# Kernel optimization log

Measured on AMD Instinct MI355X. Metric: run time of the kernel, lower is better.

Reference implementation:

```python
import jax, jax.numpy as jnp
import numpy as np

N_NODES = 100000
N_EDGES = 1600000
IN_DIM = 128
HID = 128
FC_DIM = 64
OUT_DIM = 1
NUM_LAYERS = 8
NUM_GRAPHS = 128
EPS = 1e-5


def _layernorm(x, gamma, beta):
    mu = jnp.mean(x, axis=-1, keepdims=True)
    var = jnp.mean(jnp.square(x - mu), axis=-1, keepdims=True)
    return (x - mu) * jax.lax.rsqrt(var + EPS) * gamma + beta


def _gcn_conv(x, row, col, W, b):
    # PyG GCNConv: h = X W; out[v] = sum_{(u,v)} norm(u,v) h[u] + b
    # self-loops already appended to row/col, norms precomputable per call
    n = x.shape[0]
    deg = jnp.zeros((n,), x.dtype).at[col].add(jnp.ones((row.shape[0],), x.dtype))
    dinv = jnp.where(deg > 0, jax.lax.rsqrt(deg), 0.0)
    norm = dinv[row] * dinv[col]                      # [E+N]
    h = x @ W                                         # [N, H]
    out = jnp.zeros((n, W.shape[1]), x.dtype).at[col].add(norm[:, None] * h[row])
    return out + b


def _block(x, row, col, W, b, g, be):
    return jax.nn.relu(_layernorm(_gcn_conv(x, row, col, W, b), g, be))


def setup_inputs() -> dict:
    key = jax.random.key(0)
    ks = jax.random.split(key, 16)
    x = jax.random.normal(ks[0], (N_NODES, IN_DIM), jnp.float32)
    edge_index = jax.random.randint(ks[1], (2, N_EDGES), 0, N_NODES, jnp.int32)
    batch = jnp.sort(jax.random.randint(ks[2], (N_NODES,), 0, NUM_GRAPHS, jnp.int32))

    def lin(k, fan_in, fan_out):
        s = 1.0 / np.sqrt(fan_in)
        return jax.random.uniform(k, (fan_in, fan_out), jnp.float32, -s, s)

    return {
        "x": x, "edge_index": edge_index, "batch": batch,
        "W_in": lin(ks[3], IN_DIM, HID), "b_in": jnp.zeros((HID,), jnp.float32),
        "g_in": jnp.ones((HID,), jnp.float32), "be_in": jnp.zeros((HID,), jnp.float32),
        "W_mid": lin(ks[4], HID, HID), "b_mid": jnp.zeros((HID,), jnp.float32),
        "g_mid": jnp.ones((HID,), jnp.float32), "be_mid": jnp.zeros((HID,), jnp.float32),
        "W_out": lin(ks[5], HID, HID), "b_out": jnp.zeros((HID,), jnp.float32),
        "g_out": jnp.ones((HID,), jnp.float32), "be_out": jnp.zeros((HID,), jnp.float32),
        "W1": lin(ks[6], HID, FC_DIM), "b1": jnp.zeros((FC_DIM,), jnp.float32),
        "W2": lin(ks[7], FC_DIM, OUT_DIM), "b2": jnp.zeros((OUT_DIM,), jnp.float32),
    }


def reference(x, edge_index, batch,
              W_in, b_in, g_in, be_in,
              W_mid, b_mid, g_mid, be_mid,
              W_out, b_out, g_out, be_out,
              W1, b1, W2, b2):
    n = x.shape[0]
    sl = jnp.arange(n, dtype=edge_index.dtype)
    row = jnp.concatenate([edge_index[0], sl])   # sources (+ self loops)
    col = jnp.concatenate([edge_index[1], sl])   # targets (+ self loops)

    # layer 0
    h = _block(x, row, col, W_in, b_in, g_in, be_in)
    # layers 1..num_layers-2 share middle_conv params; even idx adds residual
    for i in range(1, NUM_LAYERS - 1):
        if i % 2 == 0:
            h = _block(h, row, col, W_mid, b_mid, g_mid, be_mid) + h
        else:
            h = _block(h, row, col, W_mid, b_mid, g_mid, be_mid)
    # last layer
    h = _block(h, row, col, W_out, b_out, g_out, be_out)

    # global mean pool over batch ids
    ones = jnp.ones((n, 1), h.dtype)
    sums = jnp.zeros((NUM_GRAPHS, HID), h.dtype).at[batch].add(h)
    cnts = jnp.zeros((NUM_GRAPHS, 1), h.dtype).at[batch].add(ones)
    pooled = sums / jnp.maximum(cnts, 1.0)

    z = jax.nn.relu(pooled @ W1 + b1)            # dropout = identity (eval)
    return jax.nn.sigmoid(z @ W2 + b2)
```

## Files before the change

### kernel.cpp

```cpp
#include <hip/hip_runtime.h>
#include <hip/hip_fp16.h>

#define NN 100000
#define NE 1600000
#define DIM 128
#define NGRAPH 128
#define FCD 64

#define NBK 391
#define ECH 8192
#define NCH 196
#define ECAP 8192

typedef _Float16 half_t;
typedef _Float16 half2_t __attribute__((ext_vector_type(2)));
typedef _Float16 half4_t __attribute__((ext_vector_type(4)));
typedef _Float16 half8_t __attribute__((ext_vector_type(8)));
typedef float float4_t __attribute__((ext_vector_type(4)));

__device__ inline half2_t u2h(unsigned u) { union { unsigned u; half2_t h; } x; x.u = u; return x.h; }
__device__ inline unsigned h2u(half2_t h) { union { unsigned u; half2_t h; } x; x.h = h; return x.u; }
__device__ inline half8_t q2h8(uint4 q) { union { uint4 q; half8_t h; } x; x.q = q; return x.h; }

__global__ __launch_bounds__(256) void k_bucketA(const int* __restrict__ row,
                                                 const int* __restrict__ col,
                                                 int* __restrict__ staged,
                                                 int* __restrict__ offmat,
                                                 int* __restrict__ gtot) {
  __shared__ int hist[NBK];
  __shared__ int sc[512];
  __shared__ int off[NBK + 1];
  __shared__ int fill[NBK];
  int b = blockIdx.x, t = threadIdx.x;
  int e0 = b * ECH;
  int n = NE - e0; if (n > ECH) n = ECH;
  for (int j = t; j < NBK; j += 256) { hist[j] = 0; fill[j] = 0; }
  __syncthreads();
  for (int i = t; i < n; i += 256) atomicAdd(&hist[col[e0 + i] >> 8], 1);
  __syncthreads();
  sc[t] = (t < NBK) ? hist[t] : 0;
  sc[t + 256] = (t + 256 < NBK) ? hist[t + 256] : 0;
  __syncthreads();
  #pragma unroll
  for (int o = 1; o < 512; o <<= 1) {
    int a0 = (t >= o) ? sc[t - o] : 0;
    int a1 = (t + 256 >= o) ? sc[t + 256 - o] : 0;
    __syncthreads();
    sc[t] += a0; sc[t + 256] += a1;
    __syncthreads();
  }
  if (t == 0) off[0] = 0;
  for (int j = t; j < NBK; j += 256) off[j + 1] = sc[j];
  for (int j = t; j < NBK; j += 256) if (hist[j]) atomicAdd(&gtot[j], hist[j]);
  __syncthreads();
  for (int j = t; j < NBK + 1; j += 256) offmat[b * (NBK + 1) + j] = off[j];
  for (int i = t; i < n; i += 256) {
    int c = col[e0 + i], r = row[e0 + i];
    int bkt = c >> 8;
    int pos = off[bkt] + atomicAdd(&fill[bkt], 1);
    staged[e0 + pos] = (r << 8) | (c & 255);
  }
}

__global__ void k_bsum(const int* __restrict__ gtot, int* __restrict__ gbase,
                       int* __restrict__ rowptr) {
  __shared__ int sc[512];
  int t = threadIdx.x;
  sc[t] = (t < NBK) ? gtot[t] : 0;
  sc[t + 256] = (t + 256 < NBK) ? gtot[t + 256] : 0;
  __syncthreads();
  #pragma unroll
  for (int o = 1; o < 512; o <<= 1) {
    int a0 = (t >= o) ? sc[t - o] : 0;
    int a1 = (t + 256 >= o) ? sc[t + 256 - o] : 0;
    __syncthreads();
    sc[t] += a0; sc[t + 256] += a1;
    __syncthreads();
  }
  if (t == 0) { gbase[0] = 0; rowptr[NN] = NE; }
  for (int j = t; j < NBK; j += 256) gbase[j + 1] = sc[j];
}

__global__ __launch_bounds__(256) void k_csrB(const int* __restrict__ staged,
                                              const int* __restrict__ offmat,
                                              const int* __restrict__ gbase,
                                              int* __restrict__ rowptr,
                                              float* __restrict__ dinv,
                                              int* __restrict__ csrc) {
  __shared__ int pay[ECAP];
  __shared__ int csn[256];
  __shared__ int nhist[256];
  __shared__ int nscan[256];
  __shared__ int nb[256];
  __shared__ int nfill[256];
  int bkt = blockIdx.x, t = threadIdx.x;
  int gb = gbase[bkt];
  int off = 0, cnt = 0;
  if (t < NCH) {
    int base = t * (NBK + 1) + bkt;
    off = offmat[base];
    cnt = offmat[base + 1] - off;
  }
  csn[t] = cnt;
  __syncthreads();
  #pragma unroll
  for (int o = 1; o < 256; o <<= 1) {
    int a = (t >= o) ? csn[t - o] : 0;
    __syncthreads();
    csn[t] += a;
    __syncthreads();
  }
  int lb = csn[t] - cnt;
  int total = csn[255];
  if (t < NCH) {
    const int* src = staged + t * ECH + off;
    for (int i = 0; i < cnt; i++) pay[lb + i] = src[i];
  }
  nhist[t] = 0; nfill[t] = 0;
  __syncthreads();
  for (int i = t; i < total; i += 256) atomicAdd(&nhist[pay[i] & 255], 1);
  __syncthreads();
  nscan[t] = nhist[t];
  __syncthreads();
  #pragma unroll
  for (int o = 1; o < 256; o <<= 1) {
    int a = (t >= o) ? nscan[t - o] : 0;
    __syncthreads();
    nscan[t] += a;
    __syncthreads();
  }
  nb[t] = nscan[t] - nhist[t];
  int v = bkt * 256 + t;
  if (v < NN) {
    rowptr[v] = gb + nb[t];
    dinv[v] = rsqrtf((float)(nhist[t] + 1));
  }
  __syncthreads();
  for (int i = t; i < total; i += 256) {
    int p = pay[i];
    int cl = p & 255;
    int pos = nb[cl] + atomicAdd(&nfill[cl], 1);
    csrc[gb + pos] = p >> 8;
  }
}

__global__ void k_cvt(const float* __restrict__ x, half_t* __restrict__ Xh) {
  int i = blockIdx.x * 256 + threadIdx.x;
  if ((size_t)i * 4 < (size_t)NN * DIM) {
    float4 v = *(const float4*)&x[(size_t)i * 4];
    half4_t h; h[0] = (half_t)v.x; h[1] = (half_t)v.y; h[2] = (half_t)v.z; h[3] = (half_t)v.w;
    *(half4_t*)&Xh[(size_t)i * 4] = h;
  }
}

__global__ void k_wt(const float* __restrict__ W, half_t* __restrict__ Wt) {
  int e = blockIdx.x * 256 + threadIdx.x;
  if (e < DIM * DIM) {
    int j = e >> 7, k = e & 127;
    Wt[e] = (half_t)W[k * DIM + j];
  }
}

#define WT_DW 66
__global__ __launch_bounds__(256) void k_gemm(const half_t* __restrict__ X,
                                              const uint4* __restrict__ Wtg,
                                              const float* __restrict__ dinv,
                                              half_t* __restrict__ O) {
  __shared__ unsigned wt[DIM * WT_DW];
  __shared__ half_t outs[4][16 * 136];
  int t = threadIdx.x;
  int w = t >> 6, l = t & 63;
  #pragma unroll
  for (int i = 0; i < 8; i++) {
    int e = t + i * 256;
    int j = e >> 4, seg = e & 15;
    *(uint4*)&wt[j * WT_DW + seg * 4] = Wtg[e];
  }
  __syncthreads();
  int lr = l & 15, lk = l >> 4;
  #pragma unroll
  for (int t4 = 0; t4 < 2; t4++) {
    int n0w = blockIdx.x * 128 + w * 32 + t4 * 16;
    int nA = n0w + lr;
    uint4 a0 = make_uint4(0,0,0,0), a1 = a0, a2 = a0, a3 = a0;
    if (nA < NN) {
      const uint4* Xq = (const uint4*)&X[(size_t)nA * DIM];
      a0 = Xq[lk];  a1 = Xq[4 + lk];  a2 = Xq[8 + lk];  a3 = Xq[12 + lk];
    }
    float4_t acc[8] = {};
    #pragma unroll
    for (int jt = 0; jt < 8; jt++) {
      int bbase = (jt * 16 + lr) * WT_DW + lk * 4;
      uint4 b0 = *(const uint4*)&wt[bbase];
      uint4 b1 = *(const uint4*)&wt[bbase + 16];
      uint4 b2 = *(const uint4*)&wt[bbase + 32];
      uint4 b3 = *(const uint4*)&wt[bbase + 48];
      acc[jt] = __builtin_amdgcn_mfma_f32_16x16x32_f16(q2h8(a0), q2h8(b0), acc[jt], 0, 0, 0);
      acc[jt] = __builtin_amdgcn_mfma_f32_16x16x32_f16(q2h8(a1), q2h8(b1), acc[jt], 0, 0, 0);
      acc[jt] = __builtin_amdgcn_mfma_f32_16x16x32_f16(q2h8(a2), q2h8(b2), acc[jt], 0, 0, 0);
      acc[jt] = __builtin_amdgcn_mfma_f32_16x16x32_f16(q2h8(a3), q2h8(b3), acc[jt], 0, 0, 0);
    }
    float dv0 = dinv[min(n0w + lk * 4 + 0, NN - 1)];
    float dv1 = dinv[min(n0w + lk * 4 + 1, NN - 1)];
    float dv2 = dinv[min(n0w + lk * 4 + 2, NN - 1)];
    float dv3 = dinv[min(n0w + lk * 4 + 3, NN - 1)];
    #pragma unroll
    for (int jt = 0; jt < 8; jt++) {
      int cb = jt * 16 + lr;
      outs[w][(lk * 4 + 0) * 136 + cb] = (half_t)(acc[jt][0] * dv0);
      outs[w][(lk * 4 + 1) * 136 + cb] = (half_t)(acc[jt][1] * dv1);
      outs[w][(lk * 4 + 2) * 136 + cb] = (half_t)(acc[jt][2] * dv2);
      outs[w][(lk * 4 + 3) * 136 + cb] = (half_t)(acc[jt][3] * dv3);
    }
    #pragma unroll
    for (int q = 0; q < 4; q++) {
      int idx = l * 4 + q;
      int row = idx >> 4, seg = idx & 15;
      int n = n0w + row;
      if (n < NN) {
        uint4 o4 = *(const uint4*)&outs[w][row * 136 + seg * 8];
        *(uint4*)&O[(size_t)n * DIM + seg * 8] = o4;
      }
    }
  }
}

__global__ __launch_bounds__(256) void k_agg(const half2_t* __restrict__ Hh,
                      half2_t* __restrict__ Ah,
                      const int* __restrict__ rowptr, const int* __restrict__ csrc,
                      const float* __restrict__ dinv,
                      const float* __restrict__ bias, const float* __restrict__ gamma,
                      const float* __restrict__ beta, int res) {
  int tid = threadIdx.x;
  int lane = tid & 63;
  int v = blockIdx.x * 4 + (tid >> 6);
  int g = lane >> 4;
  int fl = lane & 15;
  int s0 = rowptr[v];
  int cnt = rowptr[v + 1] - s0;
  const uint4* Hq = (const uint4*)Hh;
  half2_t a0 = u2h(0u), a1 = u2h(0u), a2 = u2h(0u), a3 = u2h(0u);
  for (int i = g; i < cnt; i += 16) {
    int j1 = i + 4, j2 = i + 8, j3 = i + 12;
    int c1 = min(j1, cnt - 1);
    int c2 = min(j2, cnt - 1);
    int c3 = min(j3, cnt - 1);
    int e0 = csrc[s0 + i];
    int e1 = csrc[s0 + c1];
    int e2 = csrc[s0 + c2];
    int e3 = csrc[s0 + c3];
    uint4 q0 = Hq[(size_t)e0 * 16 + fl];
    uint4 q1 = Hq[(size_t)e1 * 16 + fl];
    uint4 q2 = Hq[(size_t)e2 * 16 + fl];
    uint4 q3 = Hq[(size_t)e3 * 16 + fl];
    a0 += u2h(q0.x); a1 += u2h(q0.y); a2 += u2h(q0.z); a3 += u2h(q0.w);
    if (j1 < cnt) { a0 += u2h(q1.x); a1 += u2h(q1.y); a2 += u2h(q1.z); a3 += u2h(q1.w); }
    if (j2 < cnt) { a0 += u2h(q2.x); a1 += u2h(q2.y); a2 += u2h(q2.z); a3 += u2h(q2.w); }
    if (j3 < cnt) { a0 += u2h(q3.x); a1 += u2h(q3.y); a2 += u2h(q3.z); a3 += u2h(q3.w); }
  }
  float f0 = (float)a0[0], f1 = (float)a0[1], f2 = (float)a1[0], f3 = (float)a1[1];
  float f4 = (float)a2[0], f5 = (float)a2[1], f6 = (float)a3[0], f7 = (float)a3[1];
  f0 += __shfl_xor(f0, 16); f0 += __shfl_xor(f0, 32);
  f1 += __shfl_xor(f1, 16); f1 += __shfl_xor(f1, 32);
  f2 += __shfl_xor(f2, 16); f2 += __shfl_xor(f2, 32);
  f3 += __shfl_xor(f3, 16); f3 += __shfl_xor(f3, 32);
  f4 += __shfl_xor(f4, 16); f4 += __shfl_xor(f4, 32);
  f5 += __shfl_xor(f5, 16); f5 += __shfl_xor(f5, 32);
  f6 += __shfl_xor(f6, 16); f6 += __shfl_xor(f6, 32);
  f7 += __shfl_xor(f7, 16); f7 += __shfl_xor(f7, 32);
  uint4 qs = Hq[(size_t)v * 16 + fl];
  half2_t s0h = u2h(qs.x), s1h = u2h(qs.y), s2h = u2h(qs.z), s3h = u2h(qs.w);
  f0 += (float)s0h[0]; f1 += (float)s0h[1]; f2 += (float)s1h[0]; f3 += (float)s1h[1];
  f4 += (float)s2h[0]; f5 += (float)s2h[1]; f6 += (float)s3h[0]; f7 += (float)s3h[1];
  float dv = dinv[v];
  float4 ba = *(const float4*)&bias[fl * 8];
  float4 bb = *(const float4*)&bias[fl * 8 + 4];
  f0 = f0 * dv + ba.x; f1 = f1 * dv + ba.y; f2 = f2 * dv + ba.z; f3 = f3 * dv + ba.w;
  f4 = f4 * dv + bb.x; f5 = f5 * dv + bb.y; f6 = f6 * dv + bb.z; f7 = f7 * dv + bb.w;
  float s  = ((f0 + f1) + (f2 + f3)) + ((f4 + f5) + (f6 + f7));
  float ss = ((f0 * f0 + f1 * f1) + (f2 * f2 + f3 * f3))
           + ((f4 * f4 + f5 * f5) + (f6 * f6 + f7 * f7));
  #pragma unroll
  for (int o = 1; o < 16; o <<= 1) { s += __shfl_xor(s, o); ss += __shfl_xor(ss, o); }
  float mu = s * (1.f / 128.f);
  float var = ss * (1.f / 128.f) - mu * mu;
  float rs = rsqrtf(var + 1e-5f);
  float pa = (g == 0) ? f0 : (g == 1) ? f2 : (g == 2) ? f4 : f6;
  float pb = (g == 0) ? f1 : (g == 1) ? f3 : (g == 2) ? f5 : f7;
  int fi = fl * 8 + g * 2;
  float2 g2 = *(const float2*)&gamma[fi];
  float2 e2 = *(const float2*)&beta[fi];
  float y0 = fmaxf((pa - mu) * rs * g2.x + e2.x, 0.f);
  float y1 = fmaxf((pb - mu) * rs * g2.y + e2.y, 0.f);
  half2_t* Ap = &Ah[(size_t)v * 64 + (fi >> 1)];
  if (res) { half2_t o2 = *Ap; y0 += (float)o2[0]; y1 += (float)o2[1]; }
  half2_t w; w[0] = (half_t)y0; w[1] = (half_t)y1;
  *Ap = w;
}

__global__ __launch_bounds__(64) void k_pool(const half2_t* __restrict__ Ah,
                                             const int* __restrict__ batch,
                                             float* __restrict__ sums) {
  const int CH = 64;
  int b0 = blockIdx.x * CH;
  int t = threadIdx.x;
  int nmax = NN - b0; if (nmax > CH) nmax = CH;
  __shared__ int bb[CH];
  bb[t] = (b0 + t < NN) ? batch[b0 + t] : -1;
  __syncthreads();
  int gfirst = bb[0], glast = bb[nmax - 1];
  if (gfirst == glast) {
    float p0 = 0.f, p1 = 0.f, q0 = 0.f, q1 = 0.f, r0 = 0.f, r1 = 0.f, u0 = 0.f, u1 = 0.f;
    int i = 0;
    for (; i + 4 <= nmax; i += 4) {
      half2_t h0 = Ah[(size_t)(b0 + i + 0) * 64 + t];
      half2_t h1 = Ah[(size_t)(b0 + i + 1) * 64 + t];
      half2_t h2 = Ah[(size_t)(b0 + i + 2) * 64 + t];
      half2_t h3 = Ah[(size_t)(b0 + i + 3) * 64 + t];
      p0 += (float)h0[0]; p1 += (float)h0[1];
      q0 += (float)h1[0]; q1 += (float)h1[1];
      r0 += (float)h2[0]; r1 += (float)h2[1];
      u0 += (float)h3[0]; u1 += (float)h3[1];
    }
    for (; i < nmax; ++i) {
      half2_t h = Ah[(size_t)(b0 + i) * 64 + t];
      p0 += (float)h[0]; p1 += (float)h[1];
    }
    atomicAdd(&sums[gfirst * DIM + 2 * t], (p0 + q0) + (r0 + u0));
    atomicAdd(&sums[gfirst * DIM + 2 * t + 1], (p1 + q1) + (r1 + u1));
  } else {
    float s0 = 0.f, s1 = 0.f;
    int cur = gfirst;
    for (int i = 0; i < nmax; i++) {
      int g = bb[i];
      if (g != cur) {
        atomicAdd(&sums[cur * DIM + 2 * t], s0);
        atomicAdd(&sums[cur * DIM + 2 * t + 1], s1);
        s0 = s1 = 0.f; cur = g;
      }
      half2_t h = Ah[(size_t)(b0 + i) * 64 + t];
      s0 += (float)h[0]; s1 += (float)h[1];
    }
    atomicAdd(&sums[cur * DIM + 2 * t], s0);
    atomicAdd(&sums[cur * DIM + 2 * t + 1], s1);
  }
}

__global__ void k_cnts(const int* __restrict__ batch, float* __restrict__ cnts) {
  int g = threadIdx.x;
  int lo = 0, hi = NN;
  while (lo < hi) { int mid = (lo + hi) >> 1; if (batch[mid] < g) lo = mid + 1; else hi = mid; }
  int a = lo;
  lo = 0; hi = NN;
  while (lo < hi) { int mid = (lo + hi) >> 1; if (batch[mid] < g + 1) lo = mid + 1; else hi = mid; }
  cnts[g] = (float)(lo - a);
}

__global__ void k_head(const float* __restrict__ sums, const float* __restrict__ cnts,
                       const float* __restrict__ W1, const float* __restrict__ b1,
                       const float* __restrict__ W2, const float* __restrict__ b2,
                       float* __restrict__ out) {
  int g = blockIdx.x, t = threadIdx.x;
  __shared__ float p[128];
  float ic = 1.f / fmaxf(cnts[g], 1.f);
  p[t] = sums[g * DIM + t] * ic;
  p[t + 64] = sums[g * DIM + 64 + t] * ic;
  __syncthreads();
  float z = b1[t];
  #pragma unroll 8
  for (int k = 0; k < 128; k++) z += p[k] * W1[k * FCD + t];
  z = fmaxf(z, 0.f);
  float sv = z * W2[t];
  #pragma unroll
  for (int o = 1; o < 64; o <<= 1) sv += __shfl_xor(sv, o);
  if (t == 0) out[g] = 1.f / (1.f + expf(-(sv + b2[0])));
}

extern "C" void kernel_launch(void* const* d_in, const int* in_sizes, int n_in,
                              void* d_out, int out_size, void* d_ws, size_t ws_size,
                              hipStream_t stream) {
  (void)in_sizes; (void)n_in; (void)out_size; (void)ws_size;
  const float* x     = (const float*)d_in[0];
  const int*   ei    = (const int*)d_in[1];
  const int*   batch = (const int*)d_in[2];
  const float* W_in  = (const float*)d_in[3];
  const float* b_in  = (const float*)d_in[4];
  const float* g_in  = (const float*)d_in[5];
  const float* be_in = (const float*)d_in[6];
  const float* W_mid = (const float*)d_in[7];
  const float* b_mid = (const float*)d_in[8];
  const float* g_mid = (const float*)d_in[9];
  const float* be_mid= (const float*)d_in[10];
  const float* W_out = (const float*)d_in[11];
  const float* b_out = (const float*)d_in[12];
  const float* g_out = (const float*)d_in[13];
  const float* be_out= (const float*)d_in[14];
  const float* W1    = (const float*)d_in[15];
  const float* b1    = (const float*)d_in[16];
  const float* W2    = (const float*)d_in[17];
  const float* b2    = (const float*)d_in[18];
  float* out = (float*)d_out;

  char* p = (char*)d_ws;
  auto alloc = [&](size_t bytes) {
    char* r = p;
    p += (bytes + 255) & ~(size_t)255;
    return r;
  };
  half_t* Ah     = (half_t*)alloc((size_t)NN * DIM * 2);
  half_t* Xh     = (half_t*)alloc((size_t)NN * DIM * 2);
  half_t* Bh     = (half_t*)alloc((size_t)NN * DIM * 2);
  half_t* Wt3    = (half_t*)alloc((size_t)3 * DIM * DIM * 2);
  float*  dinv   = (float*)alloc((size_t)NN * 4);
  int*    rowptr = (int*)alloc((size_t)(NN + 1) * 4);
  int*    csrc   = (int*)alloc((size_t)NE * 4);
  int*    staged = (int*)alloc((size_t)NCH * ECH * 4);
  int*    offmat = (int*)alloc((size_t)NCH * (NBK + 1) * 4);
  int*    gtot   = (int*)alloc((size_t)(NBK + 1) * 4);
  int*    gbase  = (int*)alloc((size_t)(NBK + 1) * 4);
  float*  sums   = (float*)alloc((size_t)NGRAPH * DIM * 4);
  float*  cnts   = (float*)alloc((size_t)NGRAPH * 4);

  const int* rowp = ei;
  const int* colp = ei + NE;

  hipMemsetAsync(gtot, 0, (size_t)(NBK + 1) * 4, stream);
  hipMemsetAsync(sums, 0, (size_t)NGRAPH * DIM * 4, stream);

  k_bucketA<<<NCH, 256, 0, stream>>>(rowp, colp, staged, offmat, gtot);
  k_bsum<<<1, 256, 0, stream>>>(gtot, gbase, rowptr);
  k_csrB<<<NBK, 256, 0, stream>>>(staged, offmat, gbase, rowptr, dinv, csrc);
  k_cvt<<<(NN * DIM / 4 + 255) / 256, 256, 0, stream>>>(x, Xh);
  k_wt<<<(DIM * DIM + 255) / 256, 256, 0, stream>>>(W_in,  Wt3);
  k_wt<<<(DIM * DIM + 255) / 256, 256, 0, stream>>>(W_mid, Wt3 + DIM * DIM);
  k_wt<<<(DIM * DIM + 255) / 256, 256, 0, stream>>>(W_out, Wt3 + 2 * DIM * DIM);

  int gemm_grid = (NN + 127) / 128;
  for (int l = 0; l < 8; l++) {
    const half_t* Wtl;
    const float *bl, *gl, *bel;
    if (l == 0)      { Wtl = Wt3;                 bl = b_in;  gl = g_in;  bel = be_in;  }
    else if (l == 7) { Wtl = Wt3 + 2 * DIM * DIM; bl = b_out; gl = g_out; bel = be_out; }
    else             { Wtl = Wt3 + DIM * DIM;     bl = b_mid; gl = g_mid; bel = be_mid; }
    const half_t* in = (l == 0) ? Xh : Ah;
    k_gemm<<<gemm_grid, 256, 0, stream>>>(in, (const uint4*)Wtl, dinv, Bh);
    int res = (l >= 2 && l <= 6 && (l % 2 == 0)) ? 1 : 0;
    k_agg<<<NN / 4, 256, 0, stream>>>((const half2_t*)Bh, (half2_t*)Ah,
                                      rowptr, csrc, dinv, bl, gl, bel, res);
  }

  k_pool<<<(NN + 63) / 64, 64, 0, stream>>>((const half2_t*)Ah, batch, sums);
  k_cnts<<<1, 128, 0, stream>>>(batch, cnts);
  k_head<<<NGRAPH, 64, 0, stream>>>(sums, cnts, W1, b1, W2, b2, out);
}
```

Baseline: 760.5 us.

## Fuse next layer's GEMM into aggregation kernel with ping-pong feature buffers

The aggregation+layernorm kernel now also runs the next layer's 128x128 transform on its 16 freshly computed node rows using MFMA, writing the dinv-scaled result into a ping-pong buffer. This drops the separate per-layer GEMM launch and the re-read of Ah from global memory. In exchange, blocks grow to 1024 threads, load the full 32KB weight tile into LDS for every 16 nodes, and add several block-wide syncs, which can lower occupancy of the latency-bound gather.

```diff
diff --git a/kernel.cpp b/kernel.cpp
--- a/kernel.cpp
+++ b/kernel.cpp
@@ -162,6 +162,7 @@
 }
 
 #define WT_DW 66
+
 __global__ __launch_bounds__(256) void k_gemm(const half_t* __restrict__ X,
                                               const uint4* __restrict__ Wtg,
                                               const float* __restrict__ dinv,
@@ -225,15 +226,28 @@
   }
 }
 
-__global__ __launch_bounds__(256) void k_agg(const half2_t* __restrict__ Hh,
-                      half2_t* __restrict__ Ah,
+__global__ __launch_bounds__(1024) void k_fused(const half2_t* __restrict__ Hh,
+                      half2_t* __restrict__ Ah, half_t* __restrict__ Bnext,
+                      const uint4* __restrict__ Wtg,
                       const int* __restrict__ rowptr, const int* __restrict__ csrc,
                       const float* __restrict__ dinv,
                       const float* __restrict__ bias, const float* __restrict__ gamma,
-                      const float* __restrict__ beta, int res) {
-  int tid = threadIdx.x;
-  int lane = tid & 63;
-  int v = blockIdx.x * 4 + (tid >> 6);
+                      const float* __restrict__ beta, int res, int doGemm) {
+  __shared__ unsigned wt[DIM * WT_DW];
+  __shared__ half_t S[16 * 136];
+  int t = threadIdx.x;
+  int w = t >> 6;
+  int lane = t & 63;
+  int n0 = blockIdx.x * 16;
+  int v = n0 + w;
+  if (doGemm) {
+    #pragma unroll
+    for (int i = 0; i < 2; i++) {
+      int e = t + i * 1024;
+      int j = e >> 4, seg = e & 15;
+      *(uint4*)&wt[j * WT_DW + seg * 4] = Wtg[e];
+    }
+  }
   int g = lane >> 4;
   int fl = lane & 15;
   int s0 = rowptr[v];
@@ -294,8 +308,47 @@
   float y1 = fmaxf((pb - mu) * rs * g2.y + e2.y, 0.f);
   half2_t* Ap = &Ah[(size_t)v * 64 + (fi >> 1)];
   if (res) { half2_t o2 = *Ap; y0 += (float)o2[0]; y1 += (float)o2[1]; }
-  half2_t w; w[0] = (half_t)y0; w[1] = (half_t)y1;
-  *Ap = w;
+  half2_t wv; wv[0] = (half_t)y0; wv[1] = (half_t)y1;
+  *Ap = wv;
+  if (!doGemm) return;
+  *(half2_t*)&S[w * 136 + fi] = wv;
+  __syncthreads();
+  float4_t acc = {0.f, 0.f, 0.f, 0.f};
+  int lr = lane & 15, lk = lane >> 4;
+  if (w < 8) {
+    uint4 sa0 = *(const uint4*)&S[lr * 136 +  0 + lk * 8];
+    uint4 sa1 = *(const uint4*)&S[lr * 136 + 32 + lk * 8];
+    uint4 sa2 = *(const uint4*)&S[lr * 136 + 64 + lk * 8];
+    uint4 sa3 = *(const uint4*)&S[lr * 136 + 96 + lk * 8];
+    int bbase = (w * 16 + lr) * WT_DW + lk * 4;
+    uint4 b0 = *(const uint4*)&wt[bbase];
+    uint4 b1 = *(const uint4*)&wt[bbase + 16];
+    uint4 b2 = *(const uint4*)&wt[bbase + 32];
+    uint4 b3 = *(const uint4*)&wt[bbase + 48];
+    acc = __builtin_amdgcn_mfma_f32_16x16x32_f16(q2h8(sa0), q2h8(b0), acc, 0, 0, 0);
+    acc = __builtin_amdgcn_mfma_f32_16x16x32_f16(q2h8(sa1), q2h8(b1), acc, 0, 0, 0);
+    acc = __builtin_amdgcn_mfma_f32_16x16x32_f16(q2h8(sa2), q2h8(b2), acc, 0, 0, 0);
+    acc = __builtin_amdgcn_mfma_f32_16x16x32_f16(q2h8(sa3), q2h8(b3), acc, 0, 0, 0);
+  }
+  __syncthreads();
+  if (w < 8) {
+    float dv0 = dinv[n0 + lk * 4 + 0];
+    float dv1 = dinv[n0 + lk * 4 + 1];
+    float dv2 = dinv[n0 + lk * 4 + 2];
+    float dv3 = dinv[n0 + lk * 4 + 3];
+    int cb = w * 16 + lr;
+    S[(lk * 4 + 0) * 136 + cb] = (half_t)(acc[0] * dv0);
+    S[(lk * 4 + 1) * 136 + cb] = (half_t)(acc[1] * dv1);
+    S[(lk * 4 + 2) * 136 + cb] = (half_t)(acc[2] * dv2);
+    S[(lk * 4 + 3) * 136 + cb] = (half_t)(acc[3] * dv3);
+  }
+  __syncthreads();
+  if (w < 4) {
+    int idx = w * 64 + lane;
+    int row = idx >> 4, seg = idx & 15;
+    uint4 o4 = *(const uint4*)&S[row * 136 + seg * 8];
+    *(uint4*)&Bnext[(size_t)(n0 + row) * DIM + seg * 8] = o4;
+  }
 }
 
 __global__ __launch_bounds__(64) void k_pool(const half2_t* __restrict__ Ah,
@@ -409,7 +462,8 @@
   };
   half_t* Ah     = (half_t*)alloc((size_t)NN * DIM * 2);
   half_t* Xh     = (half_t*)alloc((size_t)NN * DIM * 2);
-  half_t* Bh     = (half_t*)alloc((size_t)NN * DIM * 2);
+  half_t* Bh0    = (half_t*)alloc((size_t)NN * DIM * 2);
+  half_t* Bh1    = (half_t*)alloc((size_t)NN * DIM * 2);
   half_t* Wt3    = (half_t*)alloc((size_t)3 * DIM * DIM * 2);
   float*  dinv   = (float*)alloc((size_t)NN * 4);
   int*    rowptr = (int*)alloc((size_t)(NN + 1) * 4);
@@ -435,18 +489,21 @@
   k_wt<<<(DIM * DIM + 255) / 256, 256, 0, stream>>>(W_mid, Wt3 + DIM * DIM);
   k_wt<<<(DIM * DIM + 255) / 256, 256, 0, stream>>>(W_out, Wt3 + 2 * DIM * DIM);
 
-  int gemm_grid = (NN + 127) / 128;
+  k_gemm<<<(NN + 127) / 128, 256, 0, stream>>>(Xh, (const uint4*)Wt3, dinv, Bh0);
+
+  half_t* Bping[2] = { Bh0, Bh1 };
   for (int l = 0; l < 8; l++) {
-    const half_t* Wtl;
     const float *bl, *gl, *bel;
-    if (l == 0)      { Wtl = Wt3;                 bl = b_in;  gl = g_in;  bel = be_in;  }
-    else if (l == 7) { Wtl = Wt3 + 2 * DIM * DIM; bl = b_out; gl = g_out; bel = be_out; }
-    else             { Wtl = Wt3 + DIM * DIM;     bl = b_mid; gl = g_mid; bel = be_mid; }
-    const half_t* in = (l == 0) ? Xh : Ah;
-    k_gemm<<<gemm_grid, 256, 0, stream>>>(in, (const uint4*)Wtl, dinv, Bh);
+    if (l == 0)      { bl = b_in;  gl = g_in;  bel = be_in;  }
+    else if (l == 7) { bl = b_out; gl = g_out; bel = be_out; }
+    else             { bl = b_mid; gl = g_mid; bel = be_mid; }
     int res = (l >= 2 && l <= 6 && (l % 2 == 0)) ? 1 : 0;
-    k_agg<<<NN / 4, 256, 0, stream>>>((const half2_t*)Bh, (half2_t*)Ah,
-                                      rowptr, csrc, dinv, bl, gl, bel, res);
+    int doGemm = (l < 7) ? 1 : 0;
+    const half_t* Wnext = (l <= 5) ? (Wt3 + DIM * DIM) : (Wt3 + 2 * DIM * DIM);
+    k_fused<<<NN / 16, 1024, 0, stream>>>((const half2_t*)Bping[l & 1],
+                                          (half2_t*)Ah, Bping[(l + 1) & 1],
+                                          (const uint4*)Wnext, rowptr, csrc, dinv,
+                                          bl, gl, bel, res, doGemm);
   }
 
   k_pool<<<(NN + 63) / 64, 64, 0, stream>>>((const half2_t*)Ah, batch, sums);
```

After: 798.4 us. 1.05x slower.
